# Kernel tuning notes

Hardware: AMD Instinct MI355X
Metric: run time of the kernel (lower is better)

## Reference

```python
import jax, jax.numpy as jnp
import numpy as np

B, S, E, H = 2, 2048, 1024, 16
HD = E // H            # head_dim = 64
ROT = 64               # rotary_dim == head_dim
BASE = 10000.0


def setup_inputs() -> dict:
    key = jax.random.key(0)
    k1, k2, k3, k4, k5 = jax.random.split(key, 5)
    return {
        "x": jax.random.normal(k1, (B, S, E), dtype=jnp.float32),
        "mask": jnp.ones((B, S), dtype=jnp.int32),
        "qkv_w": jax.random.normal(k2, (3 * E, E), dtype=jnp.float32) * (1.0 / np.sqrt(E)),
        "qkv_b": jax.random.normal(k3, (3 * E,), dtype=jnp.float32) * 0.02,
        "out_w": jax.random.normal(k4, (E, E), dtype=jnp.float32) * (1.0 / np.sqrt(E)),
        "out_b": jax.random.normal(k5, (E,), dtype=jnp.float32) * 0.02,
    }


def _rotate_half(x):
    # split last dim into (even, odd) pairs and rotate 90 degrees
    x = x.reshape(*x.shape[:-1], -1, 2)
    x1, x2 = x[..., 0], x[..., 1]
    return jnp.stack((-x2, x1), axis=-1).reshape(*x.shape[:-2], -1)


def _rope_cos_sin(seq_len, rot_dim, dtype):
    inv_freq = 1.0 / (BASE ** (jnp.arange(0, rot_dim, 2, dtype=jnp.float32) / rot_dim))
    freqs = jnp.arange(seq_len, dtype=jnp.float32)[:, None] * inv_freq[None, :]  # [S, rot/2]
    cos = jnp.repeat(jnp.cos(freqs), 2, axis=-1).astype(dtype)  # [S, rot]
    sin = jnp.repeat(jnp.sin(freqs), 2, axis=-1).astype(dtype)
    return cos, sin


def reference(x, mask, qkv_w, qkv_b, out_w, out_b):
    b, s, _ = x.shape
    qkv = x @ qkv_w.T + qkv_b                      # [B,S,3E]
    q, k, v = jnp.split(qkv, 3, axis=-1)
    shape = lambda t: t.reshape(b, s, H, HD).transpose(0, 2, 1, 3)  # [B,H,S,HD]
    q, k, v = shape(q), shape(k), shape(v)

    cos, sin = _rope_cos_sin(s, ROT, q.dtype)      # [S, ROT]
    cos = cos[None, None]                          # [1,1,S,ROT]
    sin = sin[None, None]
    q_rot, q_pass = q[..., :ROT], q[..., ROT:]
    k_rot, k_pass = k[..., :ROT], k[..., ROT:]
    q = jnp.concatenate((q_rot * cos + _rotate_half(q_rot) * sin, q_pass), axis=-1)
    k = jnp.concatenate((k_rot * cos + _rotate_half(k_rot) * sin, k_pass), axis=-1)

    scale = 1.0 / np.sqrt(HD)
    scores = jnp.einsum("bhqd,bhkd->bhqk", q, k) * scale  # [B,H,S,S]
    keep = (mask != 0)[:, None, None, :]           # [B,1,1,S]
    scores = jnp.where(keep, scores, -jnp.inf)
    attn = jax.nn.softmax(scores, axis=-1)
    context = jnp.einsum("bhqk,bhkd->bhqd", attn, v)
    context = context.transpose(0, 2, 1, 3).reshape(b, s, E)
    return context @ out_w.T + out_b
```

## Files before the change

kernel.cpp:

```cpp
#include <hip/hip_runtime.h>
#include <hip/hip_bf16.h>
#include <cmath>

#define SB 2048
#define EB 1024
#define NH 16
#define HD 64
#define KLOG 0.14391156831212788f
#define QSC 0.18033688011112042f

typedef unsigned short u16;
typedef unsigned int u32;
typedef __attribute__((ext_vector_type(8))) short short8;
typedef __attribute__((ext_vector_type(4))) float f32x4;

__device__ __forceinline__ u16 f2b(float x) {
  __hip_bfloat16 h = __float2bfloat16(x);
  return *reinterpret_cast<u16*>(&h);
}

__device__ __forceinline__ float b2f(u16 v) {
  u32 x = (u32)v << 16;
  float f;
  __builtin_memcpy(&f, &x, 4);
  return f;
}

__device__ __forceinline__ u32 pkb(float lo, float hi) {
#if __has_builtin(__builtin_amdgcn_cvt_pk_bf16_f32)
  auto v = __builtin_amdgcn_cvt_pk_bf16_f32(lo, hi);
  u32 r;
  __builtin_memcpy(&r, &v, 4);
  return r;
#else
  return (u32)f2b(lo) | ((u32)f2b(hi) << 16);
#endif
}

__device__ __forceinline__ void gl_lds16(const u16* g, u16* l) {
  __builtin_amdgcn_global_load_lds(
      (const __attribute__((address_space(1))) unsigned int*)g,
      (__attribute__((address_space(3))) unsigned int*)l, 16, 0, 0);
}

#define CN1 (4096 * 1024 / 4)
#define CN2 (3072 * 1024 / 4)
#define CN3 (1024 * 1024 / 4)
#define CNS (CN1 + CN2 + CN3)
__global__ __launch_bounds__(256) void conv_all(
    const float* __restrict__ x, const float* __restrict__ w1,
    const float* __restrict__ w2, const int* __restrict__ mask,
    u16* __restrict__ xb, u16* __restrict__ wqb, u16* __restrict__ owb,
    float* __restrict__ ctab, float* __restrict__ stab,
    float* __restrict__ fbias) {
  int i = blockIdx.x * 256 + threadIdx.x;
  if (i < CNS) {
    const float* src;
    u16* dst;
    int j;
    if (i < CN1) { src = x; dst = xb; j = i; }
    else if (i < CN1 + CN2) { src = w1; dst = wqb; j = i - CN1; }
    else { src = w2; dst = owb; j = i - CN1 - CN2; }
    float4 v = ((const float4*)src)[j];
    ushort4 o;
    o.x = f2b(v.x); o.y = f2b(v.y); o.z = f2b(v.z); o.w = f2b(v.w);
    ((ushort4*)dst)[j] = o;
  } else {
    int j = i - CNS;
    if (j < SB * 32) {
      int pos = j >> 5, p = j & 31;
      float th = (float)pos * expf(-(float)(2 * p) * KLOG);
      float sn, cs;
      sincosf(th, &sn, &cs);
      ctab[j] = cs; stab[j] = sn;
    } else {
      int j2 = j - SB * 32;
      if (j2 < 2 * SB) fbias[j2] = mask[j2] ? 0.f : -1e9f;
    }
  }
}

__global__ __launch_bounds__(256) void qkv_mfma_rope(
    const u16* __restrict__ A, const u16* __restrict__ Bw,
    const float* __restrict__ bias, const float* __restrict__ ctab,
    const float* __restrict__ stab, u16* __restrict__ qb,
    u16* __restrict__ kb, u16* __restrict__ vt) {
  __shared__ u16 As[128 * 32];
  __shared__ u16 Bs[128 * 32];
  __shared__ float CS[128 * 32];
  __shared__ float SN[128 * 32];

  const int t = threadIdx.x;
  const int lane = t & 63, wv = t >> 6;
  const int l15 = lane & 15, quad = lane >> 4;
  const int wm = wv >> 1, wn = wv & 1;
  const int m0 = blockIdx.x * 128;
  const int n0 = blockIdx.y * 128;

  f32x4 acc[4][4] = {};

  for (int k0 = 0; k0 < 1024; k0 += 32) {
#pragma unroll
    for (int c = 0; c < 2; c++) {
      int r = wv * 32 + c * 16;
      const u16* ga = A + (size_t)(m0 + r + (lane >> 2)) * 1024 + k0 + (lane & 3) * 8;
      const u16* gb = Bw + (size_t)(n0 + r + (lane >> 2)) * 1024 + k0 + (lane & 3) * 8;
      gl_lds16(ga, &As[r * 32]);
      gl_lds16(gb, &Bs[r * 32]);
    }
    __syncthreads();

    short8 a[4], b[4];
#pragma unroll
    for (int mi = 0; mi < 4; mi++)
      a[mi] = *(const short8*)&As[(wm * 64 + mi * 16 + l15) * 32 + quad * 8];
#pragma unroll
    for (int ni = 0; ni < 4; ni++)
      b[ni] = *(const short8*)&Bs[(wn * 64 + ni * 16 + l15) * 32 + quad * 8];
#pragma unroll
    for (int mi = 0; mi < 4; mi++)
#pragma unroll
      for (int ni = 0; ni < 4; ni++)
        acc[mi][ni] = __builtin_amdgcn_mfma_f32_16x16x32_bf16(a[mi], b[ni], acc[mi][ni], 0, 0, 0);
    __syncthreads();
  }

  const int n_base = n0 + wn * 64;
  const int which = n_base >> 10;
  float b4[4];
#pragma unroll
  for (int ni = 0; ni < 4; ni++) b4[ni] = bias[n_base + ni * 16 + l15];

  {
    int base = (m0 & 2047) * 32;
#pragma unroll
    for (int i = 0; i < 4; i++) {
      int idx = (t + i * 256) * 4;
      *(float4*)&CS[idx] = *(const float4*)&ctab[base + idx];
      *(float4*)&SN[idx] = *(const float4*)&stab[base + idx];
    }
  }
  __syncthreads();

  const int h = (n_base & 1023) >> 6;
  const int bb = m0 >> 11;
  if (which < 2) {
    u16* dst = (which == 0) ? qb : kb;
#pragma unroll
    for (int mi = 0; mi < 4; mi++) {
#pragma unroll
      for (int r = 0; r < 4; r++) {
        int row = wm * 64 + mi * 16 + quad * 4 + r;
        int s = (m0 & 2047) + row;
        size_t obase = ((size_t)(bb * NH + h) * SB + s) * HD;
#pragma unroll
        for (int ni = 0; ni < 4; ni++) {
          float v = acc[mi][ni][r] + b4[ni];
          int d = ni * 16 + l15;
          float pv = __shfl_xor(v, 1, 64);
          float c = CS[row * 32 + (d >> 1)];
          float sn_ = SN[row * 32 + (d >> 1)];
          v = v * c + pv * ((d & 1) ? sn_ : -sn_);
          if (which == 0) v *= QSC;
          dst[obase + d] = f2b(v);
        }
      }
    }
  } else {
    size_t tbase = (size_t)(bb * NH + h) * HD;
#pragma unroll
    for (int mi = 0; mi < 4; mi++) {
      int s0 = (m0 & 2047) + wm * 64 + mi * 16 + quad * 4;
#pragma unroll
      for (int ni = 0; ni < 4; ni++) {
        int d = ni * 16 + l15;
        u32 p0 = pkb(acc[mi][ni][0] + b4[ni], acc[mi][ni][1] + b4[ni]);
        u32 p1 = pkb(acc[mi][ni][2] + b4[ni], acc[mi][ni][3] + b4[ni]);
        uint2 pk = make_uint2(p0, p1);
        *(uint2*)&vt[(tbase + d) * SB + s0] = pk;
      }
    }
  }
}

__global__ __launch_bounds__(512, 4) void attn_mfma(
    const u16* __restrict__ qb, const u16* __restrict__ kb,
    const u16* __restrict__ vt, const float* __restrict__ fbias,
    u16* __restrict__ po0, u16* __restrict__ po1, float* __restrict__ pl) {
  __shared__ u16 Ks[2][4096];
  __shared__ u16 Vt[2][4096];
  __shared__ u32 Ps2[8][16][34];

  const int bh = blockIdx.x, b = bh >> 4;
  const int q0 = blockIdx.y * 256;
  const int kz = blockIdx.z;
  const int t = threadIdx.x;
  const int lane = t & 63, wv = t >> 6;
  const int l15 = lane & 15, quad = lane >> 4;

  short8 bq[2][2];
#pragma unroll
  for (int qh = 0; qh < 2; qh++) {
    const u16* qp = qb + ((size_t)bh * SB + q0 + wv * 32 + qh * 16 + l15) * HD;
    bq[qh][0] = *(const short8*)&qp[quad * 8];
    bq[qh][1] = *(const short8*)&qp[32 + quad * 8];
  }

  const u16* kbase = kb + (size_t)bh * SB * HD + (size_t)kz * 1024 * HD;
  const u16* vbase = vt + (size_t)bh * HD * SB + kz * 1024;
  const float* fbase = fbias + b * SB + kz * 1024;

  const int srow = lane >> 3;
  const int schunk = ((lane & 7) ^ srow) * 8;
  const int fslot = quad ^ (l15 & 7);

  gl_lds16(kbase + (size_t)(wv * 8 + srow) * HD + schunk, &Ks[0][wv * 512]);
  gl_lds16(vbase + (size_t)(wv * 8 + srow) * SB + schunk, &Vt[0][wv * 512]);

  f32x4 o[2][4] = {};
  float l_i[2] = {0.f, 0.f};

  for (int kt = 0; kt < 16; kt++) {
    const int bufi = kt & 1;
    __syncthreads();

    if (kt + 1 < 16) {
      size_t ko = (size_t)(kt + 1) * 64;
      gl_lds16(kbase + (ko + wv * 8 + srow) * HD + schunk, &Ks[1 - bufi][wv * 512]);
      gl_lds16(vbase + (size_t)(wv * 8 + srow) * SB + ko + schunk, &Vt[1 - bufi][wv * 512]);
    }

    f32x4 s0[4], s1[4];
#pragma unroll
    for (int mb = 0; mb < 4; mb++) {
      const u16* kr = &Ks[bufi][(mb * 16 + l15) * 64];
      short8 a0 = *(const short8*)&kr[fslot * 8];
      short8 a1 = *(const short8*)&kr[(fslot ^ 4) * 8];
      f32x4 z0 = {}, z1 = {};
      z0 = __builtin_amdgcn_mfma_f32_16x16x32_bf16(a0, bq[0][0], z0, 0, 0, 0);
      s0[mb] = __builtin_amdgcn_mfma_f32_16x16x32_bf16(a1, bq[0][1], z0, 0, 0, 0);
      z1 = __builtin_amdgcn_mfma_f32_16x16x32_bf16(a0, bq[1][0], z1, 0, 0, 0);
      s1[mb] = __builtin_amdgcn_mfma_f32_16x16x32_bf16(a1, bq[1][1], z1, 0, 0, 0);
    }

#pragma unroll
    for (int mb = 0; mb < 4; mb++) {
      f32x4 bias4 = *(const f32x4*)&fbase[kt * 64 + mb * 16 + quad * 4];
#pragma unroll
      for (int r = 0; r < 4; r++) {
        float p0 = __builtin_amdgcn_exp2f(s0[mb][r] + bias4[r]);
        float p1 = __builtin_amdgcn_exp2f(s1[mb][r] + bias4[r]);
        s0[mb][r] = p0; l_i[0] += p0;
        s1[mb][r] = p1; l_i[1] += p1;
      }
    }

    short8 pb0[2], pb1[2];
#pragma unroll
    for (int mb = 0; mb < 4; mb++) {
      uint2 w2 = make_uint2(pkb(s0[mb][0], s0[mb][1]), pkb(s0[mb][2], s0[mb][3]));
      *(uint2*)&Ps2[wv][l15][8 * mb + 2 * quad] = w2;
    }
#pragma unroll
    for (int kk = 0; kk < 2; kk++)
      pb0[kk] = *(const short8*)&Ps2[wv][l15][kk * 16 + 4 * quad];
#pragma unroll
    for (int mb = 0; mb < 4; mb++) {
      uint2 w2 = make_uint2(pkb(s1[mb][0], s1[mb][1]), pkb(s1[mb][2], s1[mb][3]));
      *(uint2*)&Ps2[wv][l15][8 * mb + 2 * quad] = w2;
    }
#pragma unroll
    for (int kk = 0; kk < 2; kk++)
      pb1[kk] = *(const short8*)&Ps2[wv][l15][kk * 16 + 4 * quad];

#pragma unroll
    for (int nb = 0; nb < 4; nb++) {
      const u16* vr = &Vt[bufi][(nb * 16 + l15) * 64];
      short8 v0 = *(const short8*)&vr[fslot * 8];
      short8 v1 = *(const short8*)&vr[(fslot ^ 4) * 8];
      o[0][nb] = __builtin_amdgcn_mfma_f32_16x16x32_bf16(v0, pb0[0], o[0][nb], 0, 0, 0);
      o[0][nb] = __builtin_amdgcn_mfma_f32_16x16x32_bf16(v1, pb0[1], o[0][nb], 0, 0, 0);
      o[1][nb] = __builtin_amdgcn_mfma_f32_16x16x32_bf16(v0, pb1[0], o[1][nb], 0, 0, 0);
      o[1][nb] = __builtin_amdgcn_mfma_f32_16x16x32_bf16(v1, pb1[1], o[1][nb], 0, 0, 0);
    }
  }

  u16* po = kz ? po1 : po0;
#pragma unroll
  for (int qh = 0; qh < 2; qh++) {
    float l = l_i[qh];
    l += __shfl_xor(l, 16, 64);
    l += __shfl_xor(l, 32, 64);
    float linv = 1.f / fmaxf(l, 1e-30f);
    int qrow = q0 + wv * 32 + qh * 16 + l15;
    size_t base = ((size_t)bh * SB + qrow) * HD;
#pragma unroll
    for (int nb = 0; nb < 4; nb++)
#pragma unroll
      for (int pr = 0; pr < 2; pr++) {
        int d = nb * 16 + quad * 4 + 2 * pr;
        *(u32*)&po[base + d] =
            pkb(o[qh][nb][2 * pr] * linv, o[qh][nb][2 * pr + 1] * linv);
      }
    if (quad == 0) pl[kz * (32 * SB) + bh * SB + qrow] = l;
  }
}

__global__ __launch_bounds__(256) void combine(
    const u16* __restrict__ po0, const u16* __restrict__ po1,
    const float* __restrict__ pl, u16* __restrict__ ctx) {
  int i = blockIdx.x * 256 + threadIdx.x;
  int bh = i >> 16;
  int r = i & 65535;
  int qrow = r >> 5;
  int dp = r & 31;
  u32 ua = ((const u32*)po0)[i];
  u32 ub = ((const u32*)po1)[i];
  float l0 = pl[bh * SB + qrow];
  float l1 = pl[32 * SB + bh * SB + qrow];
  float rinv = 1.f / fmaxf(l0 + l1, 1e-30f);
  float w0 = l0 * rinv, w1 = l1 * rinv;
  float o0 = b2f((u16)(ua & 0xffff)) * w0 + b2f((u16)(ub & 0xffff)) * w1;
  float o1 = b2f((u16)(ua >> 16)) * w0 + b2f((u16)(ub >> 16)) * w1;
  int b = bh >> 4, h = bh & 15;
  ((u32*)ctx)[(size_t)(b * SB + qrow) * 512 + h * 32 + dp] = pkb(o0, o1);
}

__global__ __launch_bounds__(256) void out_mfma(
    const u16* __restrict__ A, const u16* __restrict__ Bw,
    const float* __restrict__ bias, float* __restrict__ out) {
  __shared__ u16 As[64 * 32];
  __shared__ u16 Bs[128 * 32];

  const int t = threadIdx.x;
  const int lane = t & 63, wv = t >> 6;
  const int l15 = lane & 15, quad = lane >> 4;
  const int wm = wv >> 1, wn = wv & 1;
  const int m0 = blockIdx.x * 64;
  const int n0 = blockIdx.y * 128;

  f32x4 acc[2][4] = {};

  for (int k0 = 0; k0 < 1024; k0 += 32) {
    {
      const u16* ga = A + (size_t)(m0 + wv * 16 + (lane >> 2)) * 1024 + k0 + (lane & 3) * 8;
      gl_lds16(ga, &As[(wv * 16) * 32]);
#pragma unroll
      for (int c = 0; c < 2; c++) {
        int r = wv * 32 + c * 16;
        const u16* gb = Bw + (size_t)(n0 + r + (lane >> 2)) * 1024 + k0 + (lane & 3) * 8;
        gl_lds16(gb, &Bs[r * 32]);
      }
    }
    __syncthreads();

    short8 a[2], b[4];
#pragma unroll
    for (int mi = 0; mi < 2; mi++)
      a[mi] = *(const short8*)&As[(wm * 32 + mi * 16 + l15) * 32 + quad * 8];
#pragma unroll
    for (int ni = 0; ni < 4; ni++)
      b[ni] = *(const short8*)&Bs[(wn * 64 + ni * 16 + l15) * 32 + quad * 8];
#pragma unroll
    for (int mi = 0; mi < 2; mi++)
#pragma unroll
      for (int ni = 0; ni < 4; ni++)
        acc[mi][ni] = __builtin_amdgcn_mfma_f32_16x16x32_bf16(a[mi], b[ni], acc[mi][ni], 0, 0, 0);
    __syncthreads();
  }

  float b4[4];
#pragma unroll
  for (int ni = 0; ni < 4; ni++) b4[ni] = bias[n0 + wn * 64 + ni * 16 + l15];
#pragma unroll
  for (int mi = 0; mi < 2; mi++)
#pragma unroll
    for (int r = 0; r < 4; r++) {
      int m = m0 + wm * 32 + mi * 16 + quad * 4 + r;
#pragma unroll
      for (int ni = 0; ni < 4; ni++)
        out[(size_t)m * 1024 + n0 + wn * 64 + ni * 16 + l15] = acc[mi][ni][r] + b4[ni];
    }
}

extern "C" void kernel_launch(void* const* d_in, const int* in_sizes, int n_in,
                              void* d_out, int out_size, void* d_ws, size_t ws_size,
                              hipStream_t stream) {
  const float* x     = (const float*)d_in[0];
  const int* mask    = (const int*)d_in[1];
  const float* qkv_w = (const float*)d_in[2];
  const float* qkv_b = (const float*)d_in[3];
  const float* out_w = (const float*)d_in[4];
  const float* out_b = (const float*)d_in[5];
  float* out = (float*)d_out;

  char* wsb = (char*)d_ws;
  u16* xb    = (u16*)wsb;
  u16* wqb   = (u16*)(wsb + ( 8ull << 20));
  u16* owb   = (u16*)(wsb + (14ull << 20));
  u16* qb    = (u16*)(wsb + (16ull << 20));
  u16* kb    = (u16*)(wsb + (24ull << 20));
  u16* vtb   = (u16*)(wsb + (32ull << 20));
  u16* cxb   = (u16*)(wsb + (40ull << 20));
  u16* po1   = (u16*)(wsb + (48ull << 20));
  float* ctab  = (float*)(wsb + (56ull << 20));
  float* stab  = (float*)(wsb + (56ull << 20) + (256u << 10));
  float* fbias = (float*)(wsb + (56ull << 20) + (512u << 10));
  float* pl    = (float*)(wsb + (56ull << 20) + (768u << 10));
  u16* po0   = xb;

  dim3 blk(256);
  int convBlocks = (CNS + SB * 32 + 2 * SB + 255) / 256;
  hipLaunchKernelGGL(conv_all, dim3(convBlocks), blk, 0, stream,
                     x, qkv_w, out_w, mask, xb, wqb, owb, ctab, stab, fbias);

  hipLaunchKernelGGL(qkv_mfma_rope, dim3(32, 24), blk, 0, stream,
                     xb, wqb, qkv_b, ctab, stab, qb, kb, vtb);

  hipLaunchKernelGGL(attn_mfma, dim3(32, 8, 2), dim3(512), 0, stream,
                     qb, kb, vtb, fbias, po0, po1, pl);

  hipLaunchKernelGGL(combine, dim3(8192), blk, 0, stream, po0, po1, pl, cxb);

  hipLaunchKernelGGL(out_mfma, dim3(64, 8), blk, 0, stream, cxb, owb, out_b, out);
}
```

Baseline: 207.1 us.

## Fuse split-K attention combine into output projection and drop rope LDS tables

Removes the separate combine kernel and instead merges the two partial attention outputs, weighted by their softmax denominators, while staging the A tile of the output projection GEMM. This saves a kernel launch and a write and read of the context buffer, but the combine work is now repeated once per N-block (8 times) and loads go through registers instead of direct global-to-LDS. The QKV kernel also stops staging the cos/sin tables in shared memory, reading them straight from global memory, and declares a launch-bounds occupancy hint of 4 blocks.

```diff
diff --git a/kernel.cpp b/kernel.cpp
--- a/kernel.cpp
+++ b/kernel.cpp
@@ -80,15 +80,13 @@
   }
 }
 
-__global__ __launch_bounds__(256) void qkv_mfma_rope(
+__global__ __launch_bounds__(256, 4) void qkv_mfma_rope(
     const u16* __restrict__ A, const u16* __restrict__ Bw,
     const float* __restrict__ bias, const float* __restrict__ ctab,
     const float* __restrict__ stab, u16* __restrict__ qb,
     u16* __restrict__ kb, u16* __restrict__ vt) {
   __shared__ u16 As[128 * 32];
   __shared__ u16 Bs[128 * 32];
-  __shared__ float CS[128 * 32];
-  __shared__ float SN[128 * 32];
 
   const int t = threadIdx.x;
   const int lane = t & 63, wv = t >> 6;
@@ -131,17 +129,6 @@
 #pragma unroll
   for (int ni = 0; ni < 4; ni++) b4[ni] = bias[n_base + ni * 16 + l15];
 
-  {
-    int base = (m0 & 2047) * 32;
-#pragma unroll
-    for (int i = 0; i < 4; i++) {
-      int idx = (t + i * 256) * 4;
-      *(float4*)&CS[idx] = *(const float4*)&ctab[base + idx];
-      *(float4*)&SN[idx] = *(const float4*)&stab[base + idx];
-    }
-  }
-  __syncthreads();
-
   const int h = (n_base & 1023) >> 6;
   const int bb = m0 >> 11;
   if (which < 2) {
@@ -153,13 +140,15 @@
         int row = wm * 64 + mi * 16 + quad * 4 + r;
         int s = (m0 & 2047) + row;
         size_t obase = ((size_t)(bb * NH + h) * SB + s) * HD;
+        const float* cp = ctab + (size_t)s * 32;
+        const float* sp = stab + (size_t)s * 32;
 #pragma unroll
         for (int ni = 0; ni < 4; ni++) {
           float v = acc[mi][ni][r] + b4[ni];
           int d = ni * 16 + l15;
           float pv = __shfl_xor(v, 1, 64);
-          float c = CS[row * 32 + (d >> 1)];
-          float sn_ = SN[row * 32 + (d >> 1)];
+          float c = cp[d >> 1];
+          float sn_ = sp[d >> 1];
           v = v * c + pv * ((d & 1) ? sn_ : -sn_);
           if (which == 0) v *= QSC;
           dst[obase + d] = f2b(v);
@@ -306,28 +295,9 @@
   }
 }
 
-__global__ __launch_bounds__(256) void combine(
+__global__ __launch_bounds__(256) void out_fused(
     const u16* __restrict__ po0, const u16* __restrict__ po1,
-    const float* __restrict__ pl, u16* __restrict__ ctx) {
-  int i = blockIdx.x * 256 + threadIdx.x;
-  int bh = i >> 16;
-  int r = i & 65535;
-  int qrow = r >> 5;
-  int dp = r & 31;
-  u32 ua = ((const u32*)po0)[i];
-  u32 ub = ((const u32*)po1)[i];
-  float l0 = pl[bh * SB + qrow];
-  float l1 = pl[32 * SB + bh * SB + qrow];
-  float rinv = 1.f / fmaxf(l0 + l1, 1e-30f);
-  float w0 = l0 * rinv, w1 = l1 * rinv;
-  float o0 = b2f((u16)(ua & 0xffff)) * w0 + b2f((u16)(ub & 0xffff)) * w1;
-  float o1 = b2f((u16)(ua >> 16)) * w0 + b2f((u16)(ub >> 16)) * w1;
-  int b = bh >> 4, h = bh & 15;
-  ((u32*)ctx)[(size_t)(b * SB + qrow) * 512 + h * 32 + dp] = pkb(o0, o1);
-}
-
-__global__ __launch_bounds__(256) void out_mfma(
-    const u16* __restrict__ A, const u16* __restrict__ Bw,
+    const float* __restrict__ pl, const u16* __restrict__ Bw,
     const float* __restrict__ bias, float* __restrict__ out) {
   __shared__ u16 As[64 * 32];
   __shared__ u16 Bs[128 * 32];
@@ -339,18 +309,40 @@
   const int m0 = blockIdx.x * 64;
   const int n0 = blockIdx.y * 128;
 
+  const int ar = t >> 2, ac = t & 3;
+  const int am = m0 + ar;
+  const int ab = am >> 11, aqrow = am & 2047;
+
   f32x4 acc[2][4] = {};
 
   for (int k0 = 0; k0 < 1024; k0 += 32) {
     {
-      const u16* ga = A + (size_t)(m0 + wv * 16 + (lane >> 2)) * 1024 + k0 + (lane & 3) * 8;
-      gl_lds16(ga, &As[(wv * 16) * 32]);
-#pragma unroll
-      for (int c = 0; c < 2; c++) {
-        int r = wv * 32 + c * 16;
-        const u16* gb = Bw + (size_t)(n0 + r + (lane >> 2)) * 1024 + k0 + (lane & 3) * 8;
-        gl_lds16(gb, &Bs[r * 32]);
+      int h = k0 >> 6;
+      int d = (k0 & 32) + ac * 8;
+      int bh = ab * 16 + h;
+      float l0 = pl[bh * SB + aqrow];
+      float l1 = pl[32 * SB + bh * SB + aqrow];
+      float rinv = 1.f / fmaxf(l0 + l1, 1e-30f);
+      float w0 = l0 * rinv, w1 = l1 * rinv;
+      size_t off = ((size_t)bh * SB + aqrow) * HD + d;
+      uint4 ua = *(const uint4*)&po0[off];
+      uint4 ub = *(const uint4*)&po1[off];
+      const u32* pa = (const u32*)&ua;
+      const u32* pq = (const u32*)&ub;
+      u32 res[4];
+#pragma unroll
+      for (int j = 0; j < 4; j++) {
+        float o0 = b2f((u16)(pa[j] & 0xffff)) * w0 + b2f((u16)(pq[j] & 0xffff)) * w1;
+        float o1 = b2f((u16)(pa[j] >> 16)) * w0 + b2f((u16)(pq[j] >> 16)) * w1;
+        res[j] = pkb(o0, o1);
       }
+      *(uint4*)&As[ar * 32 + ac * 8] = *(const uint4*)res;
+    }
+#pragma unroll
+    for (int c = 0; c < 2; c++) {
+      int r = wv * 32 + c * 16;
+      const u16* gb = Bw + (size_t)(n0 + r + (lane >> 2)) * 1024 + k0 + (lane & 3) * 8;
+      gl_lds16(gb, &Bs[r * 32]);
     }
     __syncthreads();
 
@@ -401,7 +393,6 @@
   u16* qb    = (u16*)(wsb + (16ull << 20));
   u16* kb    = (u16*)(wsb + (24ull << 20));
   u16* vtb   = (u16*)(wsb + (32ull << 20));
-  u16* cxb   = (u16*)(wsb + (40ull << 20));
   u16* po1   = (u16*)(wsb + (48ull << 20));
   float* ctab  = (float*)(wsb + (56ull << 20));
   float* stab  = (float*)(wsb + (56ull << 20) + (256u << 10));
@@ -420,7 +411,6 @@
   hipLaunchKernelGGL(attn_mfma, dim3(32, 8, 2), dim3(512), 0, stream,
                      qb, kb, vtb, fbias, po0, po1, pl);
 
-  hipLaunchKernelGGL(combine, dim3(8192), blk, 0, stream, po0, po1, pl, cxb);
-
-  hipLaunchKernelGGL(out_mfma, dim3(64, 8), blk, 0, stream, cxb, owb, out_b, out);
-}
+  hipLaunchKernelGGL(out_fused, dim3(64, 8), blk, 0, stream,
+                     po0, po1, pl, owb, out_b, out);
+}
```

Measured after the change: 197.2 us. 4.7% less time.
